# Optimization experiments

Measured on AMD Instinct MI355X. Metric: run time of the kernel, lower is better.

The kernel has to match this reference:

```python
import jax, jax.numpy as jnp
import numpy as np

B, T, C, H = 4, 2048, 1024, 16
D = C // H
EPS = 1e-5


def setup_inputs() -> dict:
    key = jax.random.key(0)
    ks = jax.random.split(key, 8)
    s = 0.02
    return {
        "hidden_states": jax.random.normal(ks[0], (B, T, C), jnp.float32),
        "w_attn": jax.random.normal(ks[1], (C, 3 * C), jnp.float32) * s,
        "b_attn": jnp.zeros((3 * C,), jnp.float32),
        "w_proj": jax.random.normal(ks[2], (C, C), jnp.float32) * s,
        "b_proj": jnp.zeros((C,), jnp.float32),
        "ln1_g": jnp.ones((C,), jnp.float32),
        "ln1_b": jnp.zeros((C,), jnp.float32),
        "ln2_g": jnp.ones((C,), jnp.float32),
        "ln2_b": jnp.zeros((C,), jnp.float32),
        "w_fc": jax.random.normal(ks[3], (C, 4 * C), jnp.float32) * s,
        "b_fc": jnp.zeros((4 * C,), jnp.float32),
        "w_fc2": jax.random.normal(ks[4], (4 * C, C), jnp.float32) * s,
        "b_fc2": jnp.zeros((C,), jnp.float32),
    }


def _layernorm(x, g, b):
    mu = jnp.mean(x, axis=-1, keepdims=True)
    var = jnp.mean(jnp.square(x - mu), axis=-1, keepdims=True)
    return (x - mu) * jax.lax.rsqrt(var + EPS) * g + b


def _attention(x, w_attn, b_attn, w_proj, b_proj):
    Bx, Tx, Cx = x.shape
    qkv = x @ w_attn + b_attn  # [B,T,3C]  (GCLinear transpose=True => x @ W)
    q, k, v = jnp.split(qkv, 3, axis=-1)
    # [B,T,C] -> [B,H,T,D]
    q = q.reshape(Bx, Tx, H, D).transpose(0, 2, 1, 3)
    k = k.reshape(Bx, Tx, H, D).transpose(0, 2, 1, 3)
    v = v.reshape(Bx, Tx, H, D).transpose(0, 2, 1, 3)
    att = jnp.einsum("bhqd,bhkd->bhqk", q, k) * (1.0 / np.sqrt(D))
    causal = jnp.tril(jnp.ones((Tx, Tx), bool))
    att = jnp.where(causal, att, -jnp.inf)
    att = jax.nn.softmax(att, axis=-1)
    y = jnp.einsum("bhqk,bhkd->bhqd", att, v)
    y = y.transpose(0, 2, 1, 3).reshape(Bx, Tx, Cx)
    return y @ w_proj + b_proj


def reference(hidden_states, w_attn, b_attn, w_proj, b_proj,
              ln1_g, ln1_b, ln2_g, ln2_b, w_fc, b_fc, w_fc2, b_fc2):
    x = hidden_states
    a = _attention(_layernorm(x, ln1_g, ln1_b), w_attn, b_attn, w_proj, b_proj)
    x = x + a
    h = _layernorm(x, ln2_g, ln2_b)
    h = jax.nn.gelu(h @ w_fc + b_fc, approximate=False)  # nn.GELU default = exact erf
    h = h @ w_fc2 + b_fc2
    return x + h
```

## Files before the change

### kernel.cpp

```cpp
#include <hip/hip_runtime.h>
#include <hip/hip_bf16.h>
#include <stdint.h>

typedef __bf16 bf16_t;
typedef __bf16 bf16x8 __attribute__((ext_vector_type(8)));
typedef __bf16 bf16x4 __attribute__((ext_vector_type(4)));
typedef float f32x4 __attribute__((ext_vector_type(4)));
typedef short short4v __attribute__((ext_vector_type(4)));

#define BDIM_B 4
#define TDIM 2048
#define CDIM 1024

__device__ __forceinline__ void gload16(const void* g, void* l) {
  using GP = const __attribute__((address_space(1))) char*;
  using LP = __attribute__((address_space(3))) char*;
  __builtin_amdgcn_global_load_lds((GP)(uintptr_t)g, (LP)(uint32_t)(uintptr_t)l, 16, 0, 0);
}

#define S_BARRIER() asm volatile("s_barrier" ::: "memory")

__global__ __launch_bounds__(256)
void transpose_cast(const float* __restrict__ W, bf16_t* __restrict__ Wt, int K, int N) {
  __shared__ float tile[32][33];
  const int tx = threadIdx.x & 31, ty = threadIdx.x >> 5;
  const int n0 = blockIdx.x * 32, k0 = blockIdx.y * 32;
#pragma unroll
  for (int j = 0; j < 32; j += 8)
    tile[ty + j][tx] = W[(size_t)(k0 + ty + j) * N + n0 + tx];
  __syncthreads();
#pragma unroll
  for (int j = 0; j < 32; j += 8)
    Wt[(size_t)(n0 + ty + j) * K + k0 + tx] = (bf16_t)tile[tx][ty + j];
}

__global__ __launch_bounds__(256)
void transpose_v(const bf16_t* __restrict__ qkv, bf16_t* __restrict__ vT) {
  __shared__ bf16_t tile[64 * 64];
  const int tt = blockIdx.x;
  const int h = blockIdx.y, b = blockIdx.z;
  const int tid = threadIdx.x;
  const int sr = tid >> 3, sc = tid & 7;
  const bf16_t* src = qkv + (size_t)(b * TDIM) * 3072 + 2048 + h * 64;
#pragma unroll
  for (int p = 0; p < 2; ++p) {
    const int t = p * 32 + sr;
    *(uint4*)(tile + t * 64 + ((sc ^ (t & 7)) * 8)) =
        *(const uint4*)(src + (size_t)(tt * 64 + t) * 3072 + sc * 8);
  }
  __syncthreads();
  const int d = tid >> 2, tq = tid & 3;
  bf16_t* dst = vT + ((size_t)((b * 16 + h) * 64 + d)) * TDIM + tt * 64;
#pragma unroll
  for (int p = 0; p < 2; ++p) {
    union { uint4 u; bf16_t e[8]; } o;
#pragma unroll
    for (int j = 0; j < 8; ++j) {
      const int t = p * 32 + tq * 8 + j;
      o.e[j] = tile[t * 64 + (((d >> 3) ^ (t & 7)) * 8) + (d & 7)];
    }
    *(uint4*)(dst + p * 32 + tq * 8) = o.u;
  }
}

__global__ __launch_bounds__(256)
void ln_kernel(const float* __restrict__ x, const float* __restrict__ g,
               const float* __restrict__ bta, bf16_t* __restrict__ out) {
  const size_t row = blockIdx.x;
  const int tid = threadIdx.x;
  const float4 v = ((const float4*)(x + row * CDIM))[tid];
  float s = v.x + v.y + v.z + v.w;
#pragma unroll
  for (int off = 1; off < 64; off <<= 1) s += __shfl_xor(s, off);
  __shared__ float r1[4], r2[4];
  const int wv = tid >> 6, lane = tid & 63;
  if (!lane) r1[wv] = s;
  __syncthreads();
  const float mu = (r1[0] + r1[1] + r1[2] + r1[3]) * (1.f / CDIM);
  const float dx = v.x - mu, dy = v.y - mu, dz = v.z - mu, dw = v.w - mu;
  float q = dx * dx + dy * dy + dz * dz + dw * dw;
#pragma unroll
  for (int off = 1; off < 64; off <<= 1) q += __shfl_xor(q, off);
  if (!lane) r2[wv] = q;
  __syncthreads();
  const float var = (r2[0] + r2[1] + r2[2] + r2[3]) * (1.f / CDIM);
  const float rs = rsqrtf(var + 1e-5f);
  const float4 gg = ((const float4*)g)[tid];
  const float4 bb = ((const float4*)bta)[tid];
  bf16x4 o;
  o[0] = (bf16_t)(dx * rs * gg.x + bb.x);
  o[1] = (bf16_t)(dy * rs * gg.y + bb.y);
  o[2] = (bf16_t)(dz * rs * gg.z + bb.z);
  o[3] = (bf16_t)(dw * rs * gg.w + bb.w);
  ((bf16x4*)(out + row * CDIM))[tid] = o;
}

enum { EPI_BF16 = 0, EPI_RESID = 1, EPI_GELU = 2 };

template <int EPI>
__global__ __launch_bounds__(512)
void gemm256(const bf16_t* __restrict__ A, const bf16_t* __restrict__ Bt,
             const float* __restrict__ bias, const float* __restrict__ resid,
             void* __restrict__ outv, int M, int N, int K) {
  __shared__ bf16_t sA[2][256 * 64];
  __shared__ bf16_t sB[2][256 * 64];
  const int tid = threadIdx.x;
  const int lane = tid & 63, wv = tid >> 6;
  const int wm = wv >> 2, wn = wv & 3;
  const int rin = lane & 15, quad = lane >> 4;

  const int nwg = gridDim.x * gridDim.y;
  const int bid = blockIdx.y * gridDim.x + blockIdx.x;
  const int swzb = (bid & 7) * (nwg >> 3) + (bid >> 3);
  const int bx = swzb % gridDim.x, by = swzb / gridDim.x;
  const int m0 = by * 256, n0 = bx * 256;

  const int c8 = (lane & 7) ^ ((lane >> 3) & 7);
  const int aRow = wm * 128 + (wv & 3) * 8 + (lane >> 3);
  const int bRow = wn * 64 + (wv >> 2) * 8 + (lane >> 3);
  const bf16_t* srcA = A + (size_t)(m0 + aRow) * K + c8 * 8;
  const bf16_t* srcB = Bt + (size_t)(n0 + bRow) * K + c8 * 8;
  const int dstA = (wm * 128 + (wv & 3) * 8) * 64;
  const int dstB = (wn * 64 + (wv >> 2) * 8) * 64;

#define STA(buf, r, kk) gload16(srcA + (size_t)(32 * (r)) * K + (kk), (buf) + dstA + 32 * (r) * 64)
#define STB(buf, r, kk) gload16(srcB + (size_t)(16 * (r)) * K + (kk), (buf) + dstB + 16 * (r) * 64)

  const int ck0 = (quad ^ (rin & 7)) * 8;
  const int ck1 = ((4 + quad) ^ (rin & 7)) * 8;
  const int aBase = (wm * 128 + rin) * 64;
  const int bBase = (wn * 64 + rin) * 64;

  f32x4 acc[8][4] = {};
  bf16x8 af[8][2], bfr[4][2];

#define RDA(mi) { af[mi][0] = *(const bf16x8*)(rA + aBase + (mi)*1024 + ck0); \
                  af[mi][1] = *(const bf16x8*)(rA + aBase + (mi)*1024 + ck1); }
#define RDB(ni) { bfr[ni][0] = *(const bf16x8*)(rB + bBase + (ni)*1024 + ck0); \
                  bfr[ni][1] = *(const bf16x8*)(rB + bBase + (ni)*1024 + ck1); }
#define MM(mi, ni) { acc[mi][ni] = __builtin_amdgcn_mfma_f32_16x16x32_bf16(af[mi][0], bfr[ni][0], acc[mi][ni], 0, 0, 0); \
                     acc[mi][ni] = __builtin_amdgcn_mfma_f32_16x16x32_bf16(af[mi][1], bfr[ni][1], acc[mi][ni], 0, 0, 0); }

  const int NT = K >> 6;

  STA(sA[0], 0, 0); STA(sA[0], 1, 0); STA(sA[0], 2, 0); STA(sA[0], 3, 0);
  STB(sB[0], 0, 0); STB(sB[0], 1, 0); STB(sB[0], 2, 0); STB(sB[0], 3, 0);
  asm volatile("s_waitcnt vmcnt(0)" ::: "memory");
  S_BARRIER();

  for (int t = 0; t < NT; ++t) {
    const bf16_t* rA = sA[t & 1];
    const bf16_t* rB = sB[t & 1];
    bf16_t* wA = sA[(t & 1) ^ 1];
    bf16_t* wB = sB[(t & 1) ^ 1];
    const int kk = (t + 1 < NT ? t + 1 : t) * 64;

    STA(wA, 0, kk); STA(wA, 1, kk); STA(wA, 2, kk); STA(wA, 3, kk);
    STB(wB, 0, kk); STB(wB, 1, kk); STB(wB, 2, kk); STB(wB, 3, kk);

    RDA(0) RDA(1) RDA(2) RDA(3) RDB(0) RDB(1)
    S_BARRIER();
    __builtin_amdgcn_s_setprio(1);
    MM(0, 0) MM(0, 1) MM(1, 0) MM(1, 1) MM(2, 0) MM(2, 1) MM(3, 0) MM(3, 1)
    __builtin_amdgcn_s_setprio(0);
    S_BARRIER();

    RDB(2) RDB(3)
    S_BARRIER();
    __builtin_amdgcn_s_setprio(1);
    MM(0, 2) MM(0, 3) MM(1, 2) MM(1, 3) MM(2, 2) MM(2, 3) MM(3, 2) MM(3, 3)
    __builtin_amdgcn_s_setprio(0);
    S_BARRIER();

    RDA(4) RDA(5) RDA(6) RDA(7)
    S_BARRIER();
    __builtin_amdgcn_s_setprio(1);
    MM(4, 0) MM(4, 1) MM(5, 0) MM(5, 1) MM(6, 0) MM(6, 1) MM(7, 0) MM(7, 1)
    __builtin_amdgcn_s_setprio(0);
    S_BARRIER();

    __builtin_amdgcn_s_setprio(1);
    MM(4, 2) MM(4, 3) MM(5, 2) MM(5, 3) MM(6, 2) MM(6, 3) MM(7, 2) MM(7, 3)
    __builtin_amdgcn_s_setprio(0);
    asm volatile("s_waitcnt vmcnt(0)" ::: "memory");
    S_BARRIER();
  }

  const int rbase = m0 + wm * 128 + quad * 4;
  const int cbase = n0 + wn * 64 + rin;
#pragma unroll
  for (int mi = 0; mi < 8; ++mi)
#pragma unroll
    for (int ni = 0; ni < 4; ++ni)
#pragma unroll
      for (int r = 0; r < 4; ++r) {
        const int m = rbase + mi * 16 + r;
        const int n = cbase + ni * 16;
        float v = acc[mi][ni][r] + bias[n];
        if (EPI == EPI_RESID) v += resid[(size_t)m * N + n];
        if (EPI == EPI_GELU) v = 0.5f * v * (1.0f + erff(v * 0.7071067811865476f));
        if (EPI == EPI_RESID)
          ((float*)outv)[(size_t)m * N + n] = v;
        else
          ((bf16_t*)outv)[(size_t)m * N + n] = (bf16_t)v;
      }
#undef STA
#undef STB
#undef RDA
#undef RDB
#undef MM
}

template <int EPI>
__global__ __launch_bounds__(512)
void gemm128(const bf16_t* __restrict__ A, const bf16_t* __restrict__ Bt,
             const float* __restrict__ bias, const float* __restrict__ resid,
             void* __restrict__ outv, int M, int N, int K) {
  __shared__ bf16_t sA[3][256 * 64];
  __shared__ bf16_t sB[3][128 * 64];
  const int tid = threadIdx.x;
  const int lane = tid & 63, wv = tid >> 6;
  const int wm = wv >> 1, wn = wv & 1;
  const int rin = lane & 15, quad = lane >> 4;

  const int nwg = gridDim.x * gridDim.y;
  const int bid = blockIdx.y * gridDim.x + blockIdx.x;
  const int swzb = (bid & 7) * (nwg >> 3) + (bid >> 3);
  const int bx = swzb % gridDim.x, by = swzb / gridDim.x;
  const int m0 = by * 256, n0 = bx * 128;

  const int c8 = (lane & 7) ^ ((lane >> 3) & 7);
  const bf16_t* srcA = A + (size_t)(m0 + 8 * wv + (lane >> 3)) * K + c8 * 8;
  const int dstA = (8 * wv) * 64;
  const bf16_t* srcB = Bt + (size_t)(n0 + (wv >> 2) * 64 + (wv & 3) * 8 + (lane >> 3)) * K + c8 * 8;
  const int dstB = ((wv >> 2) * 64 + (wv & 3) * 8) * 64;

#define STA(buf, r, kk) gload16(srcA + (size_t)(64 * (r)) * K + (kk), (buf) + dstA + 64 * (r) * 64)
#define STB(buf, r, kk) gload16(srcB + (size_t)(32 * (r)) * K + (kk), (buf) + dstB + 32 * (r) * 64)

  const int ck0 = (quad ^ (rin & 7)) * 8;
  const int ck1 = ((4 + quad) ^ (rin & 7)) * 8;
  const int aBase = (wm * 64 + rin) * 64;
  const int bBase = (wn * 64 + rin) * 64;

  f32x4 acc[4][4] = {};
  bf16x8 af[4][2], bfr[4][2];

#define RDA(mi) { af[mi][0] = *(const bf16x8*)(rA + aBase + (mi)*1024 + ck0); \
                  af[mi][1] = *(const bf16x8*)(rA + aBase + (mi)*1024 + ck1); }
#define RDB(ni) { bfr[ni][0] = *(const bf16x8*)(rB + bBase + (ni)*1024 + ck0); \
                  bfr[ni][1] = *(const bf16x8*)(rB + bBase + (ni)*1024 + ck1); }
#define MM(mi, ni) { acc[mi][ni] = __builtin_amdgcn_mfma_f32_16x16x32_bf16(af[mi][0], bfr[ni][0], acc[mi][ni], 0, 0, 0); \
                     acc[mi][ni] = __builtin_amdgcn_mfma_f32_16x16x32_bf16(af[mi][1], bfr[ni][1], acc[mi][ni], 0, 0, 0); }

  const int NT = K >> 6;

  STA(sA[0], 0, 0); STA(sA[0], 1, 0); STA(sA[0], 2, 0); STA(sA[0], 3, 0); STB(sB[0], 0, 0);
  STB(sB[0], 1, 0);
  STA(sA[1], 0, 64); STA(sA[1], 1, 64); STA(sA[1], 2, 64); STA(sA[1], 3, 64); STB(sB[1], 0, 64);
  STB(sB[1], 1, 64);
  asm volatile("s_waitcnt vmcnt(7)" ::: "memory");
  S_BARRIER();

  int rb = 0, wb = 2;
  for (int t = 0; t < NT; ++t) {
    const bf16_t* rA = sA[rb];
    const bf16_t* rB = sB[rb];
    bf16_t* wA = sA[wb];
    bf16_t* wB = sB[wb];
    const int kk = (t + 2 < NT ? t + 2 : NT - 1) * 64;

    RDA(0) RDA(1) RDA(2) RDA(3) RDB(0) RDB(1)
    asm volatile("s_waitcnt vmcnt(6)" ::: "memory");
    S_BARRIER();
    STA(wA, 0, kk); STA(wA, 1, kk); STA(wA, 2, kk); STA(wA, 3, kk); STB(wB, 0, kk);
    __builtin_amdgcn_s_setprio(1);
    MM(0, 0) MM(0, 1) MM(1, 0) MM(1, 1) MM(2, 0) MM(2, 1) MM(3, 0) MM(3, 1)
    __builtin_amdgcn_s_setprio(0);

    RDB(2) RDB(3)
    asm volatile("s_waitcnt vmcnt(6)" ::: "memory");
    S_BARRIER();
    STB(wB, 1, kk);
    __builtin_amdgcn_s_setprio(1);
    MM(0, 2) MM(0, 3) MM(1, 2) MM(1, 3) MM(2, 2) MM(2, 3) MM(3, 2) MM(3, 3)
    __builtin_amdgcn_s_setprio(0);

    rb = (rb == 2) ? 0 : rb + 1;
    wb = (wb == 2) ? 0 : wb + 1;
  }
  asm volatile("s_waitcnt vmcnt(0)" ::: "memory");

  const int rbase = m0 + wm * 64 + quad * 4;
  const int cbase = n0 + wn * 64 + rin;
#pragma unroll
  for (int mi = 0; mi < 4; ++mi)
#pragma unroll
    for (int ni = 0; ni < 4; ++ni)
#pragma unroll
      for (int r = 0; r < 4; ++r) {
        const int m = rbase + mi * 16 + r;
        const int n = cbase + ni * 16;
        float v = acc[mi][ni][r] + bias[n];
        if (EPI == EPI_RESID) v += resid[(size_t)m * N + n];
        if (EPI == EPI_GELU) v = 0.5f * v * (1.0f + erff(v * 0.7071067811865476f));
        if (EPI == EPI_RESID)
          ((float*)outv)[(size_t)m * N + n] = v;
        else
          ((bf16_t*)outv)[(size_t)m * N + n] = (bf16_t)v;
      }
#undef STA
#undef STB
#undef RDA
#undef RDB
#undef MM
}

__global__ __launch_bounds__(256)
void attn_kernel(const bf16_t* __restrict__ qkv, const bf16_t* __restrict__ vT,
                 bf16_t* __restrict__ y) {
  const int id = blockIdx.x;
  const int bx = id >> 6;
  const int h = id & 15, b = (id >> 4) & 3;
  const int tid = threadIdx.x, lane = tid & 63, wv = tid >> 6;
  const int rin = lane & 15, quad = lane >> 4;

  __shared__ bf16_t K2[2][64 * 64];
  __shared__ bf16_t V2[2][64 * 64];

  const size_t base3 = (size_t)(b * TDIM) * 3072;
  const bf16_t* Kg = qkv + base3 + 1024 + h * 64;
  const bf16_t* Vg = vT + (size_t)((b * 16 + h) * 64) * TDIM;
  const int sr = tid >> 3, sc = tid & 7;
  const int sx = (sc ^ (sr & 7)) * 8;
  const short4v ones = {(short)0x3F80, (short)0x3F80, (short)0x3F80, (short)0x3F80};

#define STAGE(bi, kt_) { \
    gload16(Kg + (size_t)((kt_) * 64 + sr) * 3072 + sx,      K2[bi] + sr * 64 + sc * 8);        \
    gload16(Kg + (size_t)((kt_) * 64 + 32 + sr) * 3072 + sx, K2[bi] + (32 + sr) * 64 + sc * 8); \
    gload16(Vg + (size_t)sr * TDIM + (kt_) * 64 + sx,        V2[bi] + sr * 64 + sc * 8);        \
    gload16(Vg + (size_t)(32 + sr) * TDIM + (kt_) * 64 + sx, V2[bi] + (32 + sr) * 64 + sc * 8); }

#pragma unroll 1
  for (int seg = 0; seg < 2; ++seg) {
    const int qt = seg ? bx : (31 - bx);
    const int q0 = qt * 64;
    const int nkt = qt + 1;

    bf16x8 aq[2];
    {
      const size_t qr = base3 + (size_t)(q0 + wv * 16 + rin) * 3072 + h * 64;
      aq[0] = *(const bf16x8*)(qkv + qr + quad * 8);
      aq[1] = *(const bf16x8*)(qkv + qr + 32 + quad * 8);
    }

    f32x4 o[4] = {};
    f32x4 ol = {};

    STAGE(0, 0)
    asm volatile("s_waitcnt vmcnt(0)" ::: "memory");
    S_BARRIER();

    for (int kt = 0; kt < nkt; ++kt) {
      const bf16_t* Kb = K2[kt & 1];
      const bf16_t* Vb = V2[kt & 1];
      if (kt + 1 < nkt) STAGE((kt + 1) & 1, kt + 1)
      f32x4 st[4] = {};
#pragma unroll
      for (int ki = 0; ki < 2; ++ki) {
#pragma unroll
        for (int kf = 0; kf < 4; ++kf) {
          const bf16x8 ak = *(const bf16x8*)(Kb + (kf * 16 + rin) * 64 +
                                             (((ki * 4 + quad) ^ (rin & 7)) * 8));
          st[kf] = __builtin_amdgcn_mfma_f32_16x16x32_bf16(ak, aq[ki], st[kf], 0, 0, 0);
        }
      }
      const bool maskt = (kt == qt);
      const int qg = q0 + wv * 16 + rin;
      short4v pf[4];
#pragma unroll
      for (int kf = 0; kf < 4; ++kf)
#pragma unroll
        for (int r = 0; r < 4; ++r) {
          const int kg = kt * 64 + kf * 16 + quad * 4 + r;
          float p = __builtin_amdgcn_exp2f(st[kf][r] * 0.18033688f);
          if (maskt && kg > qg) p = 0.f;
          union { bf16_t bv; short sv; } cv;
          cv.bv = (bf16_t)p;
          pf[kf][r] = cv.sv;
        }
#pragma unroll
      for (int kf = 0; kf < 4; ++kf) {
#pragma unroll
        for (int nd = 0; nd < 4; ++nd) {
          const short4v bv = *(const short4v*)(Vb + (nd * 16 + rin) * 64 +
                                               (((kf * 2 + (quad >> 1)) ^ (rin & 7)) * 8) +
                                               (quad & 1) * 4);
          o[nd] = __builtin_amdgcn_mfma_f32_16x16x16bf16_1k(pf[kf], bv, o[nd], 0, 0, 0);
        }
        ol = __builtin_amdgcn_mfma_f32_16x16x16bf16_1k(pf[kf], ones, ol, 0, 0, 0);
      }
      asm volatile("s_waitcnt vmcnt(0)" ::: "memory");
      S_BARRIER();
    }

#pragma unroll
    for (int r = 0; r < 4; ++r) {
      const float inv = 1.0f / ol[r];
      const size_t row = (size_t)b * TDIM + q0 + wv * 16 + quad * 4 + r;
#pragma unroll
      for (int nd = 0; nd < 4; ++nd)
        y[row * CDIM + h * 64 + nd * 16 + rin] = (bf16_t)(o[nd][r] * inv);
    }
  }
#undef STAGE
}

extern "C" void kernel_launch(void* const* d_in, const int* in_sizes, int n_in,
                              void* d_out, int out_size, void* d_ws, size_t ws_size,
                              hipStream_t stream) {
  const float* x      = (const float*)d_in[0];
  const float* w_attn = (const float*)d_in[1];
  const float* b_attn = (const float*)d_in[2];
  const float* w_proj = (const float*)d_in[3];
  const float* b_proj = (const float*)d_in[4];
  const float* ln1g   = (const float*)d_in[5];
  const float* ln1b   = (const float*)d_in[6];
  const float* ln2g   = (const float*)d_in[7];
  const float* ln2b   = (const float*)d_in[8];
  const float* w_fc   = (const float*)d_in[9];
  const float* b_fc   = (const float*)d_in[10];
  const float* w_fc2  = (const float*)d_in[11];
  const float* b_fc2  = (const float*)d_in[12];
  float* out = (float*)d_out;

  char* ws = (char*)d_ws;
  bf16_t* wTattn = (bf16_t*)(ws + 0);
  bf16_t* wTproj = (bf16_t*)(ws + 6291456);
  bf16_t* wTfc   = (bf16_t*)(ws + 8388608);
  bf16_t* wTfc2  = (bf16_t*)(ws + 16777216);
  bf16_t* xn     = (bf16_t*)(ws + 25165824);
  float*  x2     = (float*)(ws + 41943040);
  bf16_t* qkv    = (bf16_t*)(ws + 75497472);
  bf16_t* yb     = (bf16_t*)(ws + 75497472 + 50331648);
  bf16_t* hb     = (bf16_t*)(ws + 75497472);
  bf16_t* vT     = xn;

  transpose_cast<<<dim3(96, 32), 256, 0, stream>>>(w_attn, wTattn, 1024, 3072);
  transpose_cast<<<dim3(32, 32), 256, 0, stream>>>(w_proj, wTproj, 1024, 1024);
  transpose_cast<<<dim3(128, 32), 256, 0, stream>>>(w_fc, wTfc, 1024, 4096);
  transpose_cast<<<dim3(32, 128), 256, 0, stream>>>(w_fc2, wTfc2, 4096, 1024);

  ln_kernel<<<8192, 256, 0, stream>>>(x, ln1g, ln1b, xn);
  gemm128<EPI_BF16><<<dim3(24, 32), 512, 0, stream>>>(xn, wTattn, b_attn, nullptr, qkv, 8192, 3072, 1024);
  transpose_v<<<dim3(32, 16, 4), 256, 0, stream>>>(qkv, vT);
  attn_kernel<<<dim3(1024), 256, 0, stream>>>(qkv, vT, yb);
  gemm128<EPI_RESID><<<dim3(8, 32), 512, 0, stream>>>(yb, wTproj, b_proj, x, x2, 8192, 1024, 1024);
  ln_kernel<<<8192, 256, 0, stream>>>(x2, ln2g, ln2b, xn);
  gemm256<EPI_GELU><<<dim3(16, 32), 512, 0, stream>>>(xn, wTfc, b_fc, nullptr, hb, 8192, 4096, 1024);
  gemm128<EPI_RESID><<<dim3(8, 32), 512, 0, stream>>>(hb, wTfc2, b_fc2, x2, out, 8192, 1024, 4096);
}
```

Before: 494.3 us.

## Deepen gemm256 global-to-LDS prefetch to two tiles ahead with staggered loads

Restructures the gemm256 main loop so global-to-LDS loads run up to two K-tiles ahead. They are split into halves and issued at different phases of the loop, into buffer regions whose reads have already finished. The wait at the end of each iteration becomes vmcnt(6), so only the next tile's loads must land and newer loads stay in flight. The goal is to hide global memory latency behind the MFMA work. The cost is fragile ordering between buffer reuse and barriers: a mistake in the per-thread vmcnt accounting or in when a region is overwritten could cause data races.

```diff
diff --git a/kernel.cpp b/kernel.cpp
--- a/kernel.cpp
+++ b/kernel.cpp
@@ -115,16 +115,18 @@
   const int bx = swzb % gridDim.x, by = swzb / gridDim.x;
   const int m0 = by * 256, n0 = bx * 256;
 
-  const int c8 = (lane & 7) ^ ((lane >> 3) & 7);
-  const int aRow = wm * 128 + (wv & 3) * 8 + (lane >> 3);
-  const int bRow = wn * 64 + (wv >> 2) * 8 + (lane >> 3);
-  const bf16_t* srcA = A + (size_t)(m0 + aRow) * K + c8 * 8;
-  const bf16_t* srcB = Bt + (size_t)(n0 + bRow) * K + c8 * 8;
-  const int dstA = (wm * 128 + (wv & 3) * 8) * 64;
-  const int dstB = (wn * 64 + (wv >> 2) * 8) * 64;
-
-#define STA(buf, r, kk) gload16(srcA + (size_t)(32 * (r)) * K + (kk), (buf) + dstA + 32 * (r) * 64)
-#define STB(buf, r, kk) gload16(srcB + (size_t)(16 * (r)) * K + (kk), (buf) + dstB + 16 * (r) * 64)
+  const int r0 = tid >> 3, cc = tid & 7;
+  const int sxo = (cc ^ (r0 & 7)) * 8;
+  const bf16_t* gA = A + (size_t)(m0 + r0) * K + sxo;
+  const bf16_t* gB = Bt + (size_t)(n0 + r0) * K + sxo;
+  const int ldst = r0 * 64 + cc * 8;
+
+#define STGA(buf, h, kk) { \
+    gload16(gA + (size_t)((h) * 128) * K + (kk), (buf) + (h) * 128 * 64 + ldst);              \
+    gload16(gA + (size_t)((h) * 128 + 64) * K + (kk), (buf) + ((h) * 128 + 64) * 64 + ldst); }
+#define STGB(buf, h, kk) { \
+    gload16(gB + (size_t)((h) * 128) * K + (kk), (buf) + (h) * 128 * 64 + ldst);              \
+    gload16(gB + (size_t)((h) * 128 + 64) * K + (kk), (buf) + ((h) * 128 + 64) * 64 + ldst); }
 
   const int ck0 = (quad ^ (rin & 7)) * 8;
   const int ck1 = ((4 + quad) ^ (rin & 7)) * 8;
@@ -143,9 +145,12 @@
 
   const int NT = K >> 6;
 
-  STA(sA[0], 0, 0); STA(sA[0], 1, 0); STA(sA[0], 2, 0); STA(sA[0], 3, 0);
-  STB(sB[0], 0, 0); STB(sB[0], 1, 0); STB(sB[0], 2, 0); STB(sB[0], 3, 0);
-  asm volatile("s_waitcnt vmcnt(0)" ::: "memory");
+  {
+    const int k1 = (NT > 1 ? 1 : 0) * 64;
+    STGA(sA[0], 0, 0); STGB(sB[0], 0, 0); STGA(sA[0], 1, 0); STGB(sB[0], 1, 0);
+    STGB(sB[1], 0, k1); STGA(sA[1], 0, k1); STGA(sA[1], 1, k1);
+  }
+  asm volatile("s_waitcnt vmcnt(6)" ::: "memory");
   S_BARRIER();
 
   for (int t = 0; t < NT; ++t) {
@@ -153,12 +158,11 @@
     const bf16_t* rB = sB[t & 1];
     bf16_t* wA = sA[(t & 1) ^ 1];
     bf16_t* wB = sB[(t & 1) ^ 1];
-    const int kk = (t + 1 < NT ? t + 1 : t) * 64;
-
-    STA(wA, 0, kk); STA(wA, 1, kk); STA(wA, 2, kk); STA(wA, 3, kk);
-    STB(wB, 0, kk); STB(wB, 1, kk); STB(wB, 2, kk); STB(wB, 3, kk);
+    const int kk1 = (t + 1 < NT ? t + 1 : NT - 1) * 64;
+    const int kk2 = (t + 2 < NT ? t + 2 : NT - 1) * 64;
 
     RDA(0) RDA(1) RDA(2) RDA(3) RDB(0) RDB(1)
+    STGB(wB, 1, kk1);
     S_BARRIER();
     __builtin_amdgcn_s_setprio(1);
     MM(0, 0) MM(0, 1) MM(1, 0) MM(1, 1) MM(2, 0) MM(2, 1) MM(3, 0) MM(3, 1)
@@ -173,18 +177,21 @@
     S_BARRIER();
 
     RDA(4) RDA(5) RDA(6) RDA(7)
+    STGB(sB[t & 1], 0, kk2);
     S_BARRIER();
     __builtin_amdgcn_s_setprio(1);
     MM(4, 0) MM(4, 1) MM(5, 0) MM(5, 1) MM(6, 0) MM(6, 1) MM(7, 0) MM(7, 1)
     __builtin_amdgcn_s_setprio(0);
     S_BARRIER();
 
+    STGA(sA[t & 1], 0, kk2); STGA(sA[t & 1], 1, kk2);
     __builtin_amdgcn_s_setprio(1);
     MM(4, 2) MM(4, 3) MM(5, 2) MM(5, 3) MM(6, 2) MM(6, 3) MM(7, 2) MM(7, 3)
     __builtin_amdgcn_s_setprio(0);
-    asm volatile("s_waitcnt vmcnt(0)" ::: "memory");
-    S_BARRIER();
-  }
+    asm volatile("s_waitcnt vmcnt(6)" ::: "memory");
+    S_BARRIER();
+  }
+  asm volatile("s_waitcnt vmcnt(0)" ::: "memory");
 
   const int rbase = m0 + wm * 128 + quad * 4;
   const int cbase = n0 + wn * 64 + rin;
@@ -204,8 +211,8 @@
         else
           ((bf16_t*)outv)[(size_t)m * N + n] = (bf16_t)v;
       }
-#undef STA
-#undef STB
+#undef STGA
+#undef STGB
 #undef RDA
 #undef RDB
 #undef MM
```

Result: faster. 482.9 us (-2.3%).
